# Kernel optimization log

Hardware: AMD Instinct MI355X
Metric: run time of the kernel (lower is better)

## Reference

```python
import jax, jax.numpy as jnp
import numpy as np

# Production-scale 3D conv: B=4, C=64->64, 32^3 volume, 3x3x3 kernel, stride 1, pad 1.
B, CIN, COUT = 4, 64, 64
KSIZE = (3, 3, 3)
STRIDE = (1, 1, 1)
PAD = 1
SPATIAL = (32, 32, 32)


def setup_inputs() -> dict:
    key = jax.random.key(0)
    k1, k2, k3 = jax.random.split(key, 3)
    x = jax.random.normal(k1, (B, CIN) + SPATIAL, dtype=jnp.float32)
    weight = jax.random.normal(k2, (COUT, CIN) + KSIZE, dtype=jnp.float32)
    bias = jax.random.normal(k3, (COUT,), dtype=jnp.float32)
    return {"x": x, "weight": weight, "bias": bias}


def reference(x, weight, bias):
    # The original materializes all sliding-window patches via nested unfold and
    # contracts with einsum('bci...,oci->bo...'). That is exactly a standard
    # cross-correlation (torch-style conv). We express the same math as a direct
    # convolution, avoiding the O(kernel_volume) patch blowup.
    out = jax.lax.conv_general_dilated(
        x,
        weight,
        window_strides=STRIDE,
        padding=[(PAD, PAD)] * 3,
        dimension_numbers=("NCDHW", "OIDHW", "NCDHW"),
    )
    return out + bias.reshape(1, -1, 1, 1, 1)
```

## Files before the change

kernel.cpp:

```cpp
#include <hip/hip_runtime.h>
#include <hip/hip_bf16.h>

#define WS_W_OFF    0
#define WS_ZERO_OFF 221184
#define WS_XT_OFF   262144

typedef __attribute__((ext_vector_type(8))) short s16x8;
typedef __attribute__((ext_vector_type(4))) float f32x4;

#define GLOBAL_AS __attribute__((address_space(1)))
#define LDS_AS    __attribute__((address_space(3)))

__device__ __forceinline__ unsigned short f2bf(float f) {
  unsigned u = __builtin_bit_cast(unsigned, f);
  u = u + 0x7fffu + ((u >> 16) & 1u);
  return (unsigned short)(u >> 16);
}

__global__ void prep_kernel(const float* __restrict__ x,
                            const float* __restrict__ w,
                            unsigned short* __restrict__ wsw,
                            float* __restrict__ zeros,
                            unsigned short* __restrict__ xt) {
  int blk = blockIdx.x;
  if (blk < 432) {
    int t = blk * 256 + threadIdx.x;
    int tap  = t % 27;
    int cin  = (t / 27) & 63;
    int cout = t / (27 * 64);
    int h   = cin >> 5;
    int q   = (cin >> 3) & 3;
    int j   = cin & 7;
    int nf  = cout >> 4;
    int lane = q * 16 + (cout & 15);
    int dst = (((tap * 2 + h) * 4 + nf) * 64 + lane) * 8 + j;
    wsw[dst] = f2bf(w[t]);
    if (t < 64) zeros[t] = 0.0f;
  } else {
    int t  = (blk - 432) * 256 + threadIdx.x;
    int s  = t & 32767;
    int c8 = (t >> 15) & 7;
    int b  = t >> 18;
    const float* src = x + (size_t)(b * 64 + c8 * 8) * 32768 + s;
    s16x8 v;
    #pragma unroll
    for (int k = 0; k < 8; ++k) v[k] = (short)f2bf(src[(size_t)k * 32768]);
    *(s16x8*)(xt + (size_t)(b * 32768 + s) * 64 + c8 * 8) = v;
  }
}

__global__ __launch_bounds__(256, 2) void conv_kernel(const float* __restrict__ bias,
                                                      float* __restrict__ out,
                                                      const char* __restrict__ ws) {
  __shared__ __align__(16) unsigned char halo[52 * 1024];

  const int tid  = threadIdx.x;
  const int lane = tid & 63;
  const int w    = tid >> 6;
  const int logical = (blockIdx.x & 7) * 64 + (blockIdx.x >> 3);
  const int yt = logical & 7, zt = (logical >> 3) & 15, b = logical >> 7;
  const int z0 = zt * 2, y0 = yt * 4;
  const int zo  = w >> 1;
  const int yo2 = (w & 1) * 2;

  const int r15 = lane & 15;
  const int hi4 = lane >> 4;

  const int sl_sub   = lane >> 2;
  const int sl_chunk = lane & 3;

  auto stage_halo = [&](int h) {
    for (int g = w; g < 52; g += 4) {
      int pos = g * 16 + sl_sub;
      int hz = pos / 204; int rem = pos - hz * 204;
      int hy = rem / 34;  int hx = rem - hy * 34;
      int gz = z0 + hz - 1, gy = y0 + hy - 1, gx = hx - 1;
      bool inb = (pos < 816) & ((unsigned)gz < 32u) &
                 ((unsigned)gy < 32u) & ((unsigned)gx < 32u);
      int s = (gz * 32 + gy) * 32 + gx;
      int src = inb ? (WS_XT_OFF + (b * 32768 + s) * 128 + h * 64 + sl_chunk * 16)
                    : WS_ZERO_OFF;
      __builtin_amdgcn_global_load_lds(
          (const GLOBAL_AS void*)(ws + src),
          (LDS_AS void*)(&halo[g * 1024 + lane * 16]),
          16, 0, 0);
    }
  };

  const char* wsb_lane = ws + WS_W_OFF + lane * 16;

  f32x4 zero4 = {0.f, 0.f, 0.f, 0.f};
  f32x4 acc[4][4];
  #pragma unroll
  for (int mf = 0; mf < 4; ++mf)
    #pragma unroll
    for (int nf = 0; nf < 4; ++nf) acc[mf][nf] = zero4;

  s16x8 Bb[3][4];

  auto issueB = [&](int slot, int h, int tap) {
    const char* bt = wsb_lane + (tap * 2 + h) * 4096;
    asm volatile("global_load_dwordx4 %0, %1, off"             : "=v"(Bb[slot][0]) : "v"(bt));
    asm volatile("global_load_dwordx4 %0, %1, off offset:1024" : "=v"(Bb[slot][1]) : "v"(bt));
    asm volatile("global_load_dwordx4 %0, %1, off offset:2048" : "=v"(Bb[slot][2]) : "v"(bt));
    asm volatile("global_load_dwordx4 %0, %1, off offset:3072" : "=v"(Bb[slot][3]) : "v"(bt));
  };

  auto loadA = [&](s16x8* a, int tap) {
    int kd = tap / 9; int r9 = tap - kd * 9;
    int kh = r9 / 3;  int kw = r9 - kh * 3;
    int base = ((zo + kd) * 6 + (yo2 + kh)) * 34 + kw + r15;
    #pragma unroll
    for (int mf = 0; mf < 4; ++mf) {
      int pos = base + (mf >> 1) * 34 + (mf & 1) * 16;
      a[mf] = *(const s16x8*)&halo[pos * 64 + hi4 * 16];
    }
  };

  auto compute = [&](const s16x8* a, const s16x8* B) {
    #pragma unroll
    for (int mf = 0; mf < 4; ++mf)
      #pragma unroll
      for (int nf = 0; nf < 4; ++nf)
        acc[mf][nf] = __builtin_amdgcn_mfma_f32_16x16x32_bf16(
            a[mf], B[nf], acc[mf][nf], 0, 0, 0);
  };

  auto run27 = [&](int h) {
    #pragma unroll
    for (int tap = 0; tap < 27; ++tap) {
      if (tap < 25) issueB((tap + 2) % 3, h, tap + 2);
      if (tap < 25)        { asm volatile("s_waitcnt vmcnt(8)"); }
      else if (tap == 25)  { asm volatile("s_waitcnt vmcnt(4)"); }
      else                 { asm volatile("s_waitcnt vmcnt(0)"); }
      __builtin_amdgcn_sched_barrier(0x106);
      s16x8 Af[4];
      loadA(Af, tap);
      compute(Af, Bb[tap % 3]);
    }
  };

  stage_halo(0);
  issueB(0, 0, 0); issueB(1, 0, 1);
  __syncthreads();
  run27(0);

  issueB(0, 1, 0); issueB(1, 1, 1);
  __syncthreads();
  stage_halo(1);
  __syncthreads();
  run27(1);

  const int z = z0 + zo;
  #pragma unroll
  for (int nf = 0; nf < 4; ++nf) {
    int cout = nf * 16 + r15;
    float bv = bias[cout];
    #pragma unroll
    for (int mf = 0; mf < 4; ++mf) {
      int y  = y0 + yo2 + (mf >> 1);
      int x0 = (mf & 1) * 16 + 4 * hi4;
      float* orow = out + ((size_t)((b * 64 + cout) * 32 + z) * 32 + y) * 32;
      f32x4 v;
      #pragma unroll
      for (int r = 0; r < 4; ++r) v[r] = acc[mf][nf][r] + bv;
      *(f32x4*)&orow[x0] = v;
    }
  }
}

extern "C" void kernel_launch(void* const* d_in, const int* in_sizes, int n_in,
                              void* d_out, int out_size, void* d_ws, size_t ws_size,
                              hipStream_t stream) {
  const float* x    = (const float*)d_in[0];
  const float* wgt  = (const float*)d_in[1];
  const float* bias = (const float*)d_in[2];
  float* out = (float*)d_out;
  char* ws = (char*)d_ws;

  prep_kernel<<<4528, 256, 0, stream>>>(x, wgt,
                                        (unsigned short*)(ws + WS_W_OFF),
                                        (float*)(ws + WS_ZERO_OFF),
                                        (unsigned short*)(ws + WS_XT_OFF));
  conv_kernel<<<512, 256, 0, stream>>>(bias, out, ws);
}
```

Baseline: 45.38 us.

## Fuse input transpose and bf16 cast into conv halo staging

Removes the separate pass that converted the whole input tensor to a channels-last bf16 workspace copy. Each conv block now reads fp32 input directly, converts to bf16 and writes its halo into LDS through registers instead of async global-to-LDS loads. This avoids writing and re-reading an 8 MB intermediate. In exchange, halo loads become synchronous, strided per-channel fp32 reads that are re-read across overlapping halos, and they no longer overlap with the weight prefetch as the async LDS loads did.

```diff
diff --git a/kernel.cpp b/kernel.cpp
--- a/kernel.cpp
+++ b/kernel.cpp
@@ -2,8 +2,6 @@
 #include <hip/hip_bf16.h>
 
 #define WS_W_OFF    0
-#define WS_ZERO_OFF 221184
-#define WS_XT_OFF   262144
 
 typedef __attribute__((ext_vector_type(8))) short s16x8;
 typedef __attribute__((ext_vector_type(4))) float f32x4;
@@ -17,39 +15,23 @@
   return (unsigned short)(u >> 16);
 }
 
-__global__ void prep_kernel(const float* __restrict__ x,
-                            const float* __restrict__ w,
-                            unsigned short* __restrict__ wsw,
-                            float* __restrict__ zeros,
-                            unsigned short* __restrict__ xt) {
-  int blk = blockIdx.x;
-  if (blk < 432) {
-    int t = blk * 256 + threadIdx.x;
-    int tap  = t % 27;
-    int cin  = (t / 27) & 63;
-    int cout = t / (27 * 64);
-    int h   = cin >> 5;
-    int q   = (cin >> 3) & 3;
-    int j   = cin & 7;
-    int nf  = cout >> 4;
-    int lane = q * 16 + (cout & 15);
-    int dst = (((tap * 2 + h) * 4 + nf) * 64 + lane) * 8 + j;
-    wsw[dst] = f2bf(w[t]);
-    if (t < 64) zeros[t] = 0.0f;
-  } else {
-    int t  = (blk - 432) * 256 + threadIdx.x;
-    int s  = t & 32767;
-    int c8 = (t >> 15) & 7;
-    int b  = t >> 18;
-    const float* src = x + (size_t)(b * 64 + c8 * 8) * 32768 + s;
-    s16x8 v;
-    #pragma unroll
-    for (int k = 0; k < 8; ++k) v[k] = (short)f2bf(src[(size_t)k * 32768]);
-    *(s16x8*)(xt + (size_t)(b * 32768 + s) * 64 + c8 * 8) = v;
-  }
+__global__ void wprep_kernel(const float* __restrict__ w,
+                             unsigned short* __restrict__ wsw) {
+  int t = blockIdx.x * 256 + threadIdx.x;
+  int tap  = t % 27;
+  int cin  = (t / 27) & 63;
+  int cout = t / (27 * 64);
+  int h   = cin >> 5;
+  int q   = (cin >> 3) & 3;
+  int j   = cin & 7;
+  int nf  = cout >> 4;
+  int lane = q * 16 + (cout & 15);
+  int dst = (((tap * 2 + h) * 4 + nf) * 64 + lane) * 8 + j;
+  wsw[dst] = f2bf(w[t]);
 }
 
-__global__ __launch_bounds__(256, 2) void conv_kernel(const float* __restrict__ bias,
+__global__ __launch_bounds__(256, 2) void conv_kernel(const float* __restrict__ x,
+                                                      const float* __restrict__ bias,
                                                       float* __restrict__ out,
                                                       const char* __restrict__ ws) {
   __shared__ __align__(16) unsigned char halo[52 * 1024];
@@ -66,24 +48,25 @@
   const int r15 = lane & 15;
   const int hi4 = lane >> 4;
 
-  const int sl_sub   = lane >> 2;
-  const int sl_chunk = lane & 3;
-
   auto stage_halo = [&](int h) {
-    for (int g = w; g < 52; g += 4) {
-      int pos = g * 16 + sl_sub;
+    const float* xh = x + (size_t)(b * 64 + h * 32 + (lane & 3) * 8) * 32768;
+    #pragma unroll 1
+    for (int g = w; g < 51; g += 4) {
+      int pos = g * 16 + (lane >> 2);
       int hz = pos / 204; int rem = pos - hz * 204;
       int hy = rem / 34;  int hx = rem - hy * 34;
       int gz = z0 + hz - 1, gy = y0 + hy - 1, gx = hx - 1;
-      bool inb = (pos < 816) & ((unsigned)gz < 32u) &
-                 ((unsigned)gy < 32u) & ((unsigned)gx < 32u);
-      int s = (gz * 32 + gy) * 32 + gx;
-      int src = inb ? (WS_XT_OFF + (b * 32768 + s) * 128 + h * 64 + sl_chunk * 16)
-                    : WS_ZERO_OFF;
-      __builtin_amdgcn_global_load_lds(
-          (const GLOBAL_AS void*)(ws + src),
-          (LDS_AS void*)(&halo[g * 1024 + lane * 16]),
-          16, 0, 0);
+      bool inb = ((unsigned)gz < 32u) & ((unsigned)gy < 32u) &
+                 ((unsigned)gx < 32u);
+      int s = inb ? ((gz * 32 + gy) * 32 + gx) : 0;
+      const float* xb = xh + s;
+      s16x8 v;
+      #pragma unroll
+      for (int j = 0; j < 8; ++j) {
+        float f = xb[(size_t)j * 32768];
+        v[j] = inb ? (short)f2bf(f) : (short)0;
+      }
+      *(s16x8*)&halo[g * 1024 + lane * 16] = v;
     }
   };
 
@@ -178,9 +161,6 @@
   float* out = (float*)d_out;
   char* ws = (char*)d_ws;
 
-  prep_kernel<<<4528, 256, 0, stream>>>(x, wgt,
-                                        (unsigned short*)(ws + WS_W_OFF),
-                                        (float*)(ws + WS_ZERO_OFF),
-                                        (unsigned short*)(ws + WS_XT_OFF));
-  conv_kernel<<<512, 256, 0, stream>>>(bias, out, ws);
+  wprep_kernel<<<432, 256, 0, stream>>>(wgt, (unsigned short*)(ws + WS_W_OFF));
+  conv_kernel<<<512, 256, 0, stream>>>(x, bias, out, ws);
 }
```

Result: slower. 86.46 us (+90.5%).
